# Optimization experiments

Measured on AMD Instinct MI355X. Metric: run time of the kernel, lower is better.

## Reference

```python
import jax, jax.numpy as jnp
import numpy as np

N_FEATURES = 60
WINDOW = 64
N_FFT_BINS = WINDOW // 2 + 1  # 33
HIDDEN = 256
N_OUT = 3
TOTAL_IN = N_FEATURES + N_FEATURES * N_FFT_BINS  # 2040


def setup_inputs() -> dict:
    key = jax.random.key(0)
    ks = jax.random.split(key, 9)
    B, T = 4, 4096
    x = jax.random.normal(ks[0], (B, T, N_FEATURES), dtype=jnp.float32)

    def lin(k, fan_in, fan_out):
        bound = 1.0 / np.sqrt(fan_in)
        kw, kb = jax.random.split(k)
        W = jax.random.uniform(kw, (fan_in, fan_out), minval=-bound, maxval=bound, dtype=jnp.float32)
        b = jax.random.uniform(kb, (fan_out,), minval=-bound, maxval=bound, dtype=jnp.float32)
        return W, b

    W1, b1 = lin(ks[1], TOTAL_IN, HIDDEN)
    W2, b2 = lin(ks[2], HIDDEN, HIDDEN)
    W3, b3 = lin(ks[3], HIDDEN, HIDDEN // 2)
    W4, b4 = lin(ks[4], HIDDEN // 2, N_OUT)
    return {"x": x, "W1": W1, "b1": b1, "W2": W2, "b2": b2,
            "W3": W3, "b3": b3, "W4": W4, "b4": b4}


def _fft_features(x):
    # x: [B, T, F]
    B, T, F = x.shape
    half_w = WINDOW // 2
    # reflect pad along time: (half_w, half_w - 1)
    xp = jnp.pad(x, ((0, 0), (half_w, half_w - 1), (0, 0)), mode='reflect')  # [B, T+W-1, F]
    # sliding windows: [B, T, W, F] -> [B, T, F, W] (matches torch unfold layout)
    idx = jnp.arange(T)[:, None] + jnp.arange(WINDOW)[None, :]  # [T, W]
    windows = xp[:, idx, :].transpose(0, 1, 3, 2)  # [B, T, F, W]
    fft_mag = jnp.log1p(jnp.abs(jnp.fft.rfft(windows, axis=-1)))  # [B, T, F, W//2+1]
    return fft_mag.reshape(B, T, F * N_FFT_BINS)


def reference(x, W1, b1, W2, b2, W3, b3, W4, b4):
    fft_flat = _fft_features(x)
    h = jnp.concatenate([x, fft_flat], axis=-1)  # [B, T, 2040]
    h = jax.nn.relu(h @ W1 + b1)   # dropout is identity in eval mode
    h = jax.nn.relu(h @ W2 + b2)
    h = jax.nn.relu(h @ W3 + b3)
    return h @ W4 + b4             # [B, T, 3]
```

## Files before the change

kernel.cpp:

```cpp
#include <hip/hip_runtime.h>
#include <math.h>

#define T_LEN 4096
#define NF 60
#define NBINS 33
#define KPAD 2048
#define HID 256
#define NTOK 16384
#define LINE 4208

typedef _Float16 half_t;
typedef half_t half8 __attribute__((ext_vector_type(8)));
typedef half_t half4 __attribute__((ext_vector_type(4)));
typedef float f32x4 __attribute__((ext_vector_type(4)));

#define BAR_LDS() do { \
    asm volatile("s_waitcnt lgkmcnt(0)" ::: "memory"); \
    __builtin_amdgcn_s_barrier(); \
    asm volatile("" ::: "memory"); \
} while (0)

constexpr double K_PI = 3.14159265358979323846;
constexpr double tcos(double x) {
    while (x >  K_PI) x -= 2.0 * K_PI;
    while (x < -K_PI) x += 2.0 * K_PI;
    double x2 = x * x, s = 0.0, term = 1.0;
    for (int m = 0; m < 14; ++m) { s += term; term *= -x2 / ((2.0*m + 1.0) * (2.0*m + 2.0)); }
    return s;
}
struct CosTab { float v[64]; };
constexpr CosTab make_tab() {
    CosTab t{};
    for (int j = 0; j < 64; ++j) t.v[j] = (float)tcos(2.0 * K_PI * (double)j / 64.0);
    return t;
}
__device__ constexpr CosTab CTd = make_tab();

__device__ __forceinline__ float log2_1p(float x) {
    return 0.0f + __log2f(1.0f + x);
}

__global__ __launch_bounds__(256) void prep_kernel(
        const float* __restrict__ W1, const float* __restrict__ W2,
        const float* __restrict__ W3,
        half_t* __restrict__ dftH,
        half_t* __restrict__ W1T, half_t* __restrict__ W2T,
        half_t* __restrict__ W3T) {
    int i = blockIdx.x * 256 + threadIdx.x;
    if (i < 4096) {
        int row = i >> 6, n = i & 63;
        float c = (row < 33) ? CTd.v[(row * n) & 63]
                             : CTd.v[((row - 32) * n + 48) & 63];
        dftH[i] = (half_t)c;
        return;
    }
    i -= 4096;
    if (i < 256 * KPAD) {
        int gk = i & (KPAD - 1);
        float v = 0.f;
        if (gk < 2040) {
            int j = i >> 11;
            int r;
            bool isfft = true;
            if (gk < 1920) {
                int f = gk >> 5, bin = gk & 31;
                r = NF + f * NBINS + bin;
            } else if (gk < 1980) {
                r = gk - 1920; isfft = false;
            } else {
                r = NF + (gk - 1980) * NBINS + 32;
            }
            v = W1[(size_t)r * HID + j];
            if (isfft) v *= 0.69314718055994531f;
        }
        W1T[i] = (half_t)v;
        return;
    }
    i -= 256 * KPAD;
    if (i < 256 * 256) {
        int k = i & 255, j = i >> 8;
        W2T[i] = (half_t)W2[(size_t)k * HID + j];
        return;
    }
    i -= 256 * 256;
    if (i < 128 * 256) {
        int k = i & 255, j = i >> 8;
        W3T[i] = (half_t)W3[(size_t)k * 128 + j];
    }
}

__global__ __launch_bounds__(256) void xr_kernel(
        const float* __restrict__ x, half_t* __restrict__ lineG,
        half_t* __restrict__ H0) {
    if (blockIdx.x < 240) {
        const int bf = blockIdx.x;
        const int b = bf / NF, f = bf - b * NF;
        const float* xb = x + (size_t)b * T_LEN * NF + f;
        half_t* L = lineG + (size_t)bf * LINE;
        for (int j = threadIdx.x; j < LINE; j += 256) {
            int s = j - 32;
            int r = (s < 0) ? -s : ((s > T_LEN - 1) ? 2 * (T_LEN - 1) - s : s);
            L[j] = (half_t)xb[(size_t)r * NF];
        }
        return;
    }
    const int t = (blockIdx.x - 240) * 256 + threadIdx.x;
    const int b = t >> 12, tl = t & (T_LEN - 1);
    const int i = (b << 12) + ((tl & 7) << 9) + (tl >> 3);
    const float* xp = x + (size_t)t * NF;
    half_t* hp = H0 + (size_t)i * KPAD;
#pragma unroll
    for (int f4 = 0; f4 < 15; ++f4) {
        float4 v = *(const float4*)(xp + f4 * 4);
        half4 h;
        h[0] = (half_t)v.x; h[1] = (half_t)v.y;
        h[2] = (half_t)v.z; h[3] = (half_t)v.w;
        *(half4*)&hp[1920 + f4 * 4] = h;
    }
    half8 z = {};
    *(half8*)&hp[2040] = z;
}

__global__ __launch_bounds__(256) void fft_hankel(
        const half_t* __restrict__ lineG, const half_t* __restrict__ dftH,
        half_t* __restrict__ H0) {
    __shared__ half_t L[4160];
    __shared__ half_t Tt[4][16 * 36];

    const int bid = blockIdx.x;
    const int bf = bid >> 3, c = bid & 7;
    const int b = bf / NF, f = bf - b * NF;
    const int tid = threadIdx.x;
    const int lane = tid & 63, wv = tid >> 6;
    const int lr = lane & 15, lg = lane >> 4;

    half8 a[4][2];
#pragma unroll
    for (int rf = 0; rf < 4; ++rf)
#pragma unroll
        for (int ks = 0; ks < 2; ++ks)
            a[rf][ks] = *(const half8*)&dftH[(16 * rf + lr) * 64 + ks * 32 + lg * 8];

    {
        const half_t* src = lineG + (size_t)bf * LINE + c;
        for (int j = tid; j < 4152; j += 256) L[j] = src[j];
    }
    __syncthreads();

    const int i0 = (b << 12) + (c << 9);
    const int sl = wv * 128 + lr;
    const int tl = lane >> 2, q = lane & 3;

    half8 w0 = *(const half8*)&L[8 * sl + lg * 8];
    half8 w1 = *(const half8*)&L[8 * sl + 32 + lg * 8];

#pragma unroll
    for (int cs = 0; cs < 8; ++cs) {
        f32x4 dacc[4] = {};
#pragma unroll
        for (int rf = 0; rf < 4; ++rf)
            dacc[rf] = __builtin_amdgcn_mfma_f32_16x16x32_f16(a[rf][0], w0, dacc[rf], 0, 0, 0);
#pragma unroll
        for (int rf = 0; rf < 4; ++rf)
            dacc[rf] = __builtin_amdgcn_mfma_f32_16x16x32_f16(a[rf][1], w1, dacc[rf], 0, 0, 0);

        if (cs < 7) {
            const int sn = sl + (cs + 1) * 16;
            w0 = *(const half8*)&L[8 * sn + lg * 8];
            w1 = *(const half8*)&L[8 * sn + 32 + lg * 8];
        }

#pragma unroll
        for (int rf = 0; rf < 2; ++rf) {
            half4 h4;
#pragma unroll
            for (int r = 0; r < 4; ++r) {
                float re = dacc[rf][r];
                float im = dacc[rf + 2][r];
                float v = (rf == 0 && r == 0)
                    ? ((lg == 0) ? log2_1p(fabsf(re))
                                 : log2_1p(sqrtf(re * re + im * im)))
                    : log2_1p(sqrtf(re * re + im * im));
                h4[r] = (half_t)v;
            }
            *(half4*)&Tt[wv][lr * 36 + rf * 16 + lg * 4] = h4;
        }
        asm volatile("s_waitcnt lgkmcnt(0)" ::: "memory");
        {
            half8 rowv = *(const half8*)&Tt[wv][tl * 36 + q * 8];
            const int gtok = i0 + wv * 128 + cs * 16 + tl;
            *(half8*)&H0[(size_t)gtok * KPAD + f * 32 + q * 8] = rowv;
        }
        if (lg == 0)
            H0[(size_t)(i0 + sl + cs * 16) * KPAD + 1980 + f] =
                (half_t)log2_1p(fabsf(dacc[2][0]));
    }
}

template<int BN>
__global__ __launch_bounds__(256, 2) void gemm_pipe(
        const half_t* __restrict__ A, int lda,
        const half_t* __restrict__ BT, int ldb,
        const float* __restrict__ bias,
        half_t* __restrict__ Ch, int N, int K) {
    constexpr int NFR = BN / 64;
    __shared__ half_t As[2][64 * 64];

    const int tid  = threadIdx.x;
    const int row0 = blockIdx.x * 64;
    const int col0 = blockIdx.y * BN;
    const int wv = tid >> 6, lane = tid & 63;
    const int lr = lane & 15, lg = lane >> 4;

    const int srow = tid >> 2, sg = (tid & 3) * 2;
    const int wo0 = srow * 64 + ((sg ^ (srow & 7)) * 8);
    const int wo1 = srow * 64 + (((sg + 1) ^ (srow & 7)) * 8);
    const half_t* ap = A + (size_t)(row0 + srow) * lda + sg * 8;

    const half_t* bp[NFR];
#pragma unroll
    for (int nf = 0; nf < NFR; ++nf)
        bp[nf] = BT + (size_t)(col0 + wv * (16 * NFR) + nf * 16 + lr) * ldb + lg * 8;

    f32x4 acc[4][NFR] = {};
    const int NIT = K / 64;

    half8 bcur[2][NFR], bnxt[2][NFR];
    half8 pa0, pa1, pb0, pb1;

    {
        half8 v0 = *(const half8*)(ap);
        half8 v1 = *(const half8*)(ap + 8);
        *(half8*)&As[0][wo0] = v0;
        *(half8*)&As[0][wo1] = v1;
    }
    if (NIT > 1) { pa0 = *(const half8*)(ap + 64);  pa1 = *(const half8*)(ap + 72); }
    if (NIT > 2) { pb0 = *(const half8*)(ap + 128); pb1 = *(const half8*)(ap + 136); }
#pragma unroll
    for (int ks = 0; ks < 2; ++ks)
#pragma unroll
        for (int nf = 0; nf < NFR; ++nf)
            bcur[ks][nf] = *(const half8*)(bp[nf] + ks * 32);

    for (int it = 0; it < NIT; it += 2) {
        BAR_LDS();
        if (it + 1 < NIT) {
#pragma unroll
            for (int ks = 0; ks < 2; ++ks)
#pragma unroll
                for (int nf = 0; nf < NFR; ++nf)
                    bnxt[ks][nf] = *(const half8*)(bp[nf] + (it + 1) * 64 + ks * 32);
        }
#pragma unroll
        for (int ks = 0; ks < 2; ++ks) {
            half8 af[4];
#pragma unroll
            for (int mf = 0; mf < 4; ++mf)
                af[mf] = *(const half8*)&As[0][(mf * 16 + lr) * 64 + (((ks * 4 + lg) ^ (lr & 7)) * 8)];
#pragma unroll
            for (int mf = 0; mf < 4; ++mf)
#pragma unroll
                for (int nf = 0; nf < NFR; ++nf)
                    acc[mf][nf] = __builtin_amdgcn_mfma_f32_16x16x32_f16(af[mf], bcur[ks][nf], acc[mf][nf], 0, 0, 0);
        }
        if (it + 1 < NIT) { *(half8*)&As[1][wo0] = pa0; *(half8*)&As[1][wo1] = pa1; }
        if (it + 3 < NIT) { pa0 = *(const half8*)(ap + (it + 3) * 64); pa1 = *(const half8*)(ap + (it + 3) * 64 + 8); }
        if (it + 1 >= NIT) break;

        BAR_LDS();
        if (it + 2 < NIT) {
#pragma unroll
            for (int ks = 0; ks < 2; ++ks)
#pragma unroll
                for (int nf = 0; nf < NFR; ++nf)
                    bcur[ks][nf] = *(const half8*)(bp[nf] + (it + 2) * 64 + ks * 32);
        }
#pragma unroll
        for (int ks = 0; ks < 2; ++ks) {
            half8 af[4];
#pragma unroll
            for (int mf = 0; mf < 4; ++mf)
                af[mf] = *(const half8*)&As[1][(mf * 16 + lr) * 64 + (((ks * 4 + lg) ^ (lr & 7)) * 8)];
#pragma unroll
            for (int mf = 0; mf < 4; ++mf)
#pragma unroll
                for (int nf = 0; nf < NFR; ++nf)
                    acc[mf][nf] = __builtin_amdgcn_mfma_f32_16x16x32_f16(af[mf], bnxt[ks][nf], acc[mf][nf], 0, 0, 0);
        }
        if (it + 2 < NIT) { *(half8*)&As[0][wo0] = pb0; *(half8*)&As[0][wo1] = pb1; }
        if (it + 4 < NIT) { pb0 = *(const half8*)(ap + (it + 4) * 64); pb1 = *(const half8*)(ap + (it + 4) * 64 + 8); }
    }

#pragma unroll
    for (int nf = 0; nf < NFR; ++nf) {
        int col = col0 + wv * (16 * NFR) + nf * 16 + lr;
        float bs = bias[col];
#pragma unroll
        for (int mf = 0; mf < 4; ++mf)
#pragma unroll
            for (int r = 0; r < 4; ++r) {
                int row = row0 + mf * 16 + lg * 4 + r;
                Ch[(size_t)row * N + col] = (half_t)fmaxf(acc[mf][nf][r] + bs, 0.f);
            }
    }
}

__global__ __launch_bounds__(256) void gemm3_head(
        const half_t* __restrict__ A, const half_t* __restrict__ BT,
        const float* __restrict__ b3, const float* __restrict__ W4,
        const float* __restrict__ b4, float* __restrict__ out) {
    constexpr int NFR = 2, NIT = 4;
    __shared__ half_t As[2][64 * 64];
    __shared__ float Hs[64][132];
    __shared__ float W4s[384];

    const int tid  = threadIdx.x;
    const int row0 = blockIdx.x * 64;
    const int wv = tid >> 6, lane = tid & 63;
    const int lr = lane & 15, lg = lane >> 4;

    for (int i = tid; i < 384; i += 256) W4s[i] = W4[i];

    const int srow = tid >> 2, sg = (tid & 3) * 2;
    const int wo0 = srow * 64 + ((sg ^ (srow & 7)) * 8);
    const int wo1 = srow * 64 + (((sg + 1) ^ (srow & 7)) * 8);
    const half_t* ap = A + (size_t)(row0 + srow) * 256 + sg * 8;

    const half_t* bp[NFR];
#pragma unroll
    for (int nf = 0; nf < NFR; ++nf)
        bp[nf] = BT + (size_t)(wv * 32 + nf * 16 + lr) * 256 + lg * 8;

    f32x4 acc[4][NFR] = {};
    half8 bcur[2][NFR], bnxt[2][NFR];
    half8 pa0, pa1, pb0, pb1;

    {
        half8 v0 = *(const half8*)(ap);
        half8 v1 = *(const half8*)(ap + 8);
        *(half8*)&As[0][wo0] = v0;
        *(half8*)&As[0][wo1] = v1;
    }
    pa0 = *(const half8*)(ap + 64);  pa1 = *(const half8*)(ap + 72);
    pb0 = *(const half8*)(ap + 128); pb1 = *(const half8*)(ap + 136);
#pragma unroll
    for (int ks = 0; ks < 2; ++ks)
#pragma unroll
        for (int nf = 0; nf < NFR; ++nf)
            bcur[ks][nf] = *(const half8*)(bp[nf] + ks * 32);

    for (int it = 0; it < NIT; it += 2) {
        __syncthreads();
        if (it + 1 < NIT) {
#pragma unroll
            for (int ks = 0; ks < 2; ++ks)
#pragma unroll
                for (int nf = 0; nf < NFR; ++nf)
                    bnxt[ks][nf] = *(const half8*)(bp[nf] + (it + 1) * 64 + ks * 32);
        }
#pragma unroll
        for (int ks = 0; ks < 2; ++ks) {
            half8 af[4];
#pragma unroll
            for (int mf = 0; mf < 4; ++mf)
                af[mf] = *(const half8*)&As[0][(mf * 16 + lr) * 64 + (((ks * 4 + lg) ^ (lr & 7)) * 8)];
#pragma unroll
            for (int mf = 0; mf < 4; ++mf)
#pragma unroll
                for (int nf = 0; nf < NFR; ++nf)
                    acc[mf][nf] = __builtin_amdgcn_mfma_f32_16x16x32_f16(af[mf], bcur[ks][nf], acc[mf][nf], 0, 0, 0);
        }
        if (it + 1 < NIT) { *(half8*)&As[1][wo0] = pa0; *(half8*)&As[1][wo1] = pa1; }
        if (it + 3 < NIT) { pa0 = *(const half8*)(ap + (it + 3) * 64); pa1 = *(const half8*)(ap + (it + 3) * 64 + 8); }
        if (it + 1 >= NIT) break;

        __syncthreads();
        if (it + 2 < NIT) {
#pragma unroll
            for (int ks = 0; ks < 2; ++ks)
#pragma unroll
                for (int nf = 0; nf < NFR; ++nf)
                    bcur[ks][nf] = *(const half8*)(bp[nf] + (it + 2) * 64 + ks * 32);
        }
#pragma unroll
        for (int ks = 0; ks < 2; ++ks) {
            half8 af[4];
#pragma unroll
            for (int mf = 0; mf < 4; ++mf)
                af[mf] = *(const half8*)&As[1][(mf * 16 + lr) * 64 + (((ks * 4 + lg) ^ (lr & 7)) * 8)];
#pragma unroll
            for (int mf = 0; mf < 4; ++mf)
#pragma unroll
                for (int nf = 0; nf < NFR; ++nf)
                    acc[mf][nf] = __builtin_amdgcn_mfma_f32_16x16x32_f16(af[mf], bnxt[ks][nf], acc[mf][nf], 0, 0, 0);
        }
        if (it + 2 < NIT) { *(half8*)&As[0][wo0] = pb0; *(half8*)&As[0][wo1] = pb1; }
        if (it + 4 < NIT) { pb0 = *(const half8*)(ap + (it + 4) * 64); pb1 = *(const half8*)(ap + (it + 4) * 64 + 8); }
    }

#pragma unroll
    for (int nf = 0; nf < NFR; ++nf) {
        int col = wv * 32 + nf * 16 + lr;
        float bs = b3[col];
#pragma unroll
        for (int mf = 0; mf < 4; ++mf)
#pragma unroll
            for (int r = 0; r < 4; ++r)
                Hs[mf * 16 + lg * 4 + r][col] = fmaxf(acc[mf][nf][r] + bs, 0.f);
    }
    __syncthreads();

    const int row = tid >> 2, q = tid & 3;
    float a0 = 0.f, a1 = 0.f, a2 = 0.f;
#pragma unroll
    for (int k = 0; k < 32; ++k) {
        float hv = Hs[row][q * 32 + k];
        a0 = fmaf(hv, W4s[(q * 32 + k) * 3 + 0], a0);
        a1 = fmaf(hv, W4s[(q * 32 + k) * 3 + 1], a1);
        a2 = fmaf(hv, W4s[(q * 32 + k) * 3 + 2], a2);
    }
    a0 += __shfl_xor(a0, 1); a0 += __shfl_xor(a0, 2);
    a1 += __shfl_xor(a1, 1); a1 += __shfl_xor(a1, 2);
    a2 += __shfl_xor(a2, 1); a2 += __shfl_xor(a2, 2);
    if (q == 0) {
        const int i = row0 + row;
        const int b = i >> 12, c = (i >> 9) & 7, s = i & 511;
        const int t = (b << 12) + (s << 3) + c;
        float* o = out + (size_t)t * 3;
        o[0] = a0 + b4[0]; o[1] = a1 + b4[1]; o[2] = a2 + b4[2];
    }
}

extern "C" void kernel_launch(void* const* d_in, const int* in_sizes, int n_in,
                              void* d_out, int out_size, void* d_ws, size_t ws_size,
                              hipStream_t stream) {
    (void)in_sizes; (void)n_in; (void)out_size; (void)ws_size;
    const float* x  = (const float*)d_in[0];
    const float* W1 = (const float*)d_in[1];
    const float* b1 = (const float*)d_in[2];
    const float* W2 = (const float*)d_in[3];
    const float* b2 = (const float*)d_in[4];
    const float* W3 = (const float*)d_in[5];
    const float* b3 = (const float*)d_in[6];
    const float* W4 = (const float*)d_in[7];
    const float* b4 = (const float*)d_in[8];
    float* out = (float*)d_out;

    char* w = (char*)d_ws;
    half_t* H0    = (half_t*)(w);
    half_t* H1    = (half_t*)(w + (size_t)64 * 1024 * 1024);
    half_t* H2    = (half_t*)(w + (size_t)72 * 1024 * 1024);
    half_t* W1T   = (half_t*)(w + (size_t)88 * 1024 * 1024);
    half_t* W2T   = (half_t*)(w + (size_t)89 * 1024 * 1024);
    half_t* W3T   = W2T + 256 * 256;
    half_t* dftH  = W3T + 128 * 256;
    half_t* lineG = (half_t*)(w + (size_t)90 * 1024 * 1024);

    prep_kernel<<<2448, 256, 0, stream>>>(W1, W2, W3, dftH, W1T, W2T, W3T);
    xr_kernel<<<304, 256, 0, stream>>>(x, lineG, H0);
    fft_hankel<<<240 * 8, 256, 0, stream>>>(lineG, dftH, H0);

    gemm_pipe<128><<<dim3(NTOK / 64, 2), 256, 0, stream>>>(
        H0, KPAD, W1T, KPAD, b1, H1, HID, KPAD);
    gemm_pipe<128><<<dim3(NTOK / 64, 2), 256, 0, stream>>>(
        H1, HID, W2T, HID, b2, H2, HID, HID);
    gemm3_head<<<NTOK / 64, 256, 0, stream>>>(H2, W3T, b3, W4, b4, out);
}
```

Measured before the change: 102.8 us.

## Use 128x128 tiles with 512-thread blocks for the first layer GEMM

Adds a new GEMM kernel for the large K=2048 first layer that uses 128-row by 128-column output tiles computed by 8 waves (2x4 wave grid) instead of 64-row tiles with 4 waves. Each A tile loaded into LDS is now reused across more waves, which cuts global and LDS traffic per output element. The cost is only 256 blocks at one block per CU, which reduces occupancy and latency hiding on a large-CU device. It also drops a redundant zero-add in the log helper.

```diff
diff --git a/kernel.cpp b/kernel.cpp
--- a/kernel.cpp
+++ b/kernel.cpp
@@ -37,7 +37,7 @@
 __device__ constexpr CosTab CTd = make_tab();
 
 __device__ __forceinline__ float log2_1p(float x) {
-    return 0.0f + __log2f(1.0f + x);
+    return __log2f(1.0f + x);
 }
 
 __global__ __launch_bounds__(256) void prep_kernel(
@@ -197,6 +197,113 @@
     }
 }
 
+__global__ __launch_bounds__(512, 1) void gemm_pipe512(
+        const half_t* __restrict__ A, int lda,
+        const half_t* __restrict__ BT, int ldb,
+        const float* __restrict__ bias,
+        half_t* __restrict__ Ch, int N, int K) {
+    __shared__ half_t As[2][128 * 64];
+
+    const int tid  = threadIdx.x;
+    const int row0 = blockIdx.x * 128;
+    const int col0 = blockIdx.y * 128;
+    const int wv = tid >> 6, lane = tid & 63;
+    const int lr = lane & 15, lg = lane >> 4;
+    const int wr = wv >> 2, wc = wv & 3;
+
+    const int srow = tid >> 2, sg = (tid & 3) * 2;
+    const int wo0 = srow * 64 + ((sg ^ (srow & 7)) * 8);
+    const int wo1 = srow * 64 + (((sg + 1) ^ (srow & 7)) * 8);
+    const half_t* ap = A + (size_t)(row0 + srow) * lda + sg * 8;
+
+    const half_t* bp[2];
+#pragma unroll
+    for (int nf = 0; nf < 2; ++nf)
+        bp[nf] = BT + (size_t)(col0 + wc * 32 + nf * 16 + lr) * ldb + lg * 8;
+
+    f32x4 acc[4][2] = {};
+    const int NIT = K / 64;
+
+    half8 bcur[2][2], bnxt[2][2];
+    half8 pa0, pa1, pb0, pb1;
+
+    {
+        half8 v0 = *(const half8*)(ap);
+        half8 v1 = *(const half8*)(ap + 8);
+        *(half8*)&As[0][wo0] = v0;
+        *(half8*)&As[0][wo1] = v1;
+    }
+    if (NIT > 1) { pa0 = *(const half8*)(ap + 64);  pa1 = *(const half8*)(ap + 72); }
+    if (NIT > 2) { pb0 = *(const half8*)(ap + 128); pb1 = *(const half8*)(ap + 136); }
+#pragma unroll
+    for (int ks = 0; ks < 2; ++ks)
+#pragma unroll
+        for (int nf = 0; nf < 2; ++nf)
+            bcur[ks][nf] = *(const half8*)(bp[nf] + ks * 32);
+
+    for (int it = 0; it < NIT; it += 2) {
+        BAR_LDS();
+        if (it + 1 < NIT) {
+#pragma unroll
+            for (int ks = 0; ks < 2; ++ks)
+#pragma unroll
+                for (int nf = 0; nf < 2; ++nf)
+                    bnxt[ks][nf] = *(const half8*)(bp[nf] + (it + 1) * 64 + ks * 32);
+        }
+#pragma unroll
+        for (int ks = 0; ks < 2; ++ks) {
+            half8 af[4];
+#pragma unroll
+            for (int mf = 0; mf < 4; ++mf)
+                af[mf] = *(const half8*)&As[0][(wr * 64 + mf * 16 + lr) * 64 + (((ks * 4 + lg) ^ (lr & 7)) * 8)];
+#pragma unroll
+            for (int mf = 0; mf < 4; ++mf)
+#pragma unroll
+                for (int nf = 0; nf < 2; ++nf)
+                    acc[mf][nf] = __builtin_amdgcn_mfma_f32_16x16x32_f16(af[mf], bcur[ks][nf], acc[mf][nf], 0, 0, 0);
+        }
+        if (it + 1 < NIT) { *(half8*)&As[1][wo0] = pa0; *(half8*)&As[1][wo1] = pa1; }
+        if (it + 3 < NIT) { pa0 = *(const half8*)(ap + (it + 3) * 64); pa1 = *(const half8*)(ap + (it + 3) * 64 + 8); }
+        if (it + 1 >= NIT) break;
+
+        BAR_LDS();
+        if (it + 2 < NIT) {
+#pragma unroll
+            for (int ks = 0; ks < 2; ++ks)
+#pragma unroll
+                for (int nf = 0; nf < 2; ++nf)
+                    bcur[ks][nf] = *(const half8*)(bp[nf] + (it + 2) * 64 + ks * 32);
+        }
+#pragma unroll
+        for (int ks = 0; ks < 2; ++ks) {
+            half8 af[4];
+#pragma unroll
+            for (int mf = 0; mf < 4; ++mf)
+                af[mf] = *(const half8*)&As[1][(wr * 64 + mf * 16 + lr) * 64 + (((ks * 4 + lg) ^ (lr & 7)) * 8)];
+#pragma unroll
+            for (int mf = 0; mf < 4; ++mf)
+#pragma unroll
+                for (int nf = 0; nf < 2; ++nf)
+                    acc[mf][nf] = __builtin_amdgcn_mfma_f32_16x16x32_f16(af[mf], bnxt[ks][nf], acc[mf][nf], 0, 0, 0);
+        }
+        if (it + 2 < NIT) { *(half8*)&As[0][wo0] = pb0; *(half8*)&As[0][wo1] = pb1; }
+        if (it + 4 < NIT) { pb0 = *(const half8*)(ap + (it + 4) * 64); pb1 = *(const half8*)(ap + (it + 4) * 64 + 8); }
+    }
+
+#pragma unroll
+    for (int nf = 0; nf < 2; ++nf) {
+        int col = col0 + wc * 32 + nf * 16 + lr;
+        float bs = bias[col];
+#pragma unroll
+        for (int mf = 0; mf < 4; ++mf)
+#pragma unroll
+            for (int r = 0; r < 4; ++r) {
+                int row = row0 + wr * 64 + mf * 16 + lg * 4 + r;
+                Ch[(size_t)row * N + col] = (half_t)fmaxf(acc[mf][nf][r] + bs, 0.f);
+            }
+    }
+}
+
 template<int BN>
 __global__ __launch_bounds__(256, 2) void gemm_pipe(
         const half_t* __restrict__ A, int lda,
@@ -460,7 +567,7 @@
     xr_kernel<<<304, 256, 0, stream>>>(x, lineG, H0);
     fft_hankel<<<240 * 8, 256, 0, stream>>>(lineG, dftH, H0);
 
-    gemm_pipe<128><<<dim3(NTOK / 64, 2), 256, 0, stream>>>(
+    gemm_pipe512<<<dim3(NTOK / 128, 2), 512, 0, stream>>>(
         H0, KPAD, W1T, KPAD, b1, H1, HID, KPAD);
     gemm_pipe<128><<<dim3(NTOK / 64, 2), 256, 0, stream>>>(
         H1, HID, W2T, HID, b2, H2, HID, HID);
```

Result: slower. 108.3 us (+5.4%).
